# Optimization experiments

Measured on AMD Instinct MI355X. Metric: run time of the kernel, lower is better.

The kernel has to match this reference:

```python
import jax, jax.numpy as jnp
import numpy as np

CLAMP = 1000.0


def setup_inputs() -> dict:
    key = jax.random.key(0)
    k1, k2 = jax.random.split(key)
    B, C, H, W = 1, 32, 160, 320
    left = jax.random.normal(k1, (B, C, H, W), dtype=jnp.float32)
    right = jax.random.normal(k2, (B, C, H, W), dtype=jnp.float32)
    return {"left": left, "right": right, "num_disparities": 64}


def reference(left, right, num_disparities):
    # Left cost volume (is_right=False):
    #   out[b,c,d,h,w] = left[b,c,h,w] * right[b,c,h,w-d]  if w >= d else 0
    orig_dtype = left.dtype
    l = left.astype(jnp.float32)
    r = right.astype(jnp.float32)
    B, C, H, W = l.shape
    d = jnp.arange(num_disparities)[:, None]          # (D, 1)
    w = jnp.arange(W)[None, :]                        # (1, W)
    idx = w - d                                       # (D, W)
    valid = idx >= 0                                  # (D, W)
    # Gather shifted right features: (B, C, H, D, W) -> (B, C, D, H, W)
    rg = r[..., jnp.clip(idx, 0, W - 1)]
    rg = jnp.transpose(rg, (0, 1, 3, 2, 4))
    vol = l[:, :, None, :, :] * rg                    # (B, C, D, H, W)
    vol = jnp.where(valid[None, None, :, None, :], vol, jnp.float32(0))
    return jnp.clip(vol, -CLAMP, CLAMP).astype(orig_dtype)
```

## Files before the change

kernel.cpp:

```cpp
#include <hip/hip_runtime.h>


typedef float fx4 __attribute__((ext_vector_type(4)));

constexpr float CLAMPV = 1000.0f;
constexpr int C   = 32;
constexpr int H   = 160;
constexpr int W   = 320;
constexpr int W4  = 80;
constexpr int TH  = 4;
constexpr int BLOCK = TH * W4;
constexpr int PAD = 16;
constexpr int RS  = PAD + W4;

__device__ __forceinline__ fx4 clamp4(fx4 l, fx4 r) {
    fx4 o;
    o.x = fminf(fmaxf(l.x * r.x, -CLAMPV), CLAMPV);
    o.y = fminf(fmaxf(l.y * r.y, -CLAMPV), CLAMPV);
    o.z = fminf(fmaxf(l.z * r.z, -CLAMPV), CLAMPV);
    o.w = fminf(fmaxf(l.w * r.w, -CLAMPV), CLAMPV);
    return o;
}

template<int O>
__device__ __forceinline__ fx4 shuf(const fx4 A, const fx4 B) {
    if constexpr (O == 0) {
        return A;
    } else if constexpr (O == 1) {
        fx4 r = {A.y, A.z, A.w, B.x}; return r;
    } else if constexpr (O == 2) {
        fx4 r = {A.z, A.w, B.x, B.y}; return r;
    } else {
        fx4 r = {A.w, B.x, B.y, B.z}; return r;
    }
}

template<int C0>
__device__ __forceinline__ void group(const fx4* __restrict__ Ab, const fx4 l,
                                      float* __restrict__ ob, int w4, int D,
                                      size_t DSTRIDE) {
    constexpr int O = (4 - (C0 & 3)) & 3;
    const int kmax = (D - C0 + 3) >> 2;
    float* p = ob + (size_t)C0 * DSTRIDE;
    int qa = w4 - (C0 ? 1 : 0);
    for (int k = 0; k < kmax; ++k, --qa, p += 4 * DSTRIDE) {
        const fx4 A = Ab[qa];
        fx4 r;
        if constexpr (O == 0) {
            r = A;
        } else {
            const fx4 B = Ab[qa + 1];
            r = shuf<O>(A, B);
        }
        const fx4 o = clamp4(l, r);
        __builtin_nontemporal_store(o, reinterpret_cast<fx4*>(p));
    }
}

__global__ __launch_bounds__(BLOCK) void costvol_kernel(
    const float* __restrict__ left,
    const float* __restrict__ right,
    float* __restrict__ out,
    int D)
{
    const int blk = blockIdx.x;
    const int c   = blk / (H / TH);
    const int h0  = (blk - c * (H / TH)) * TH;

    __shared__ fx4 sR[TH * RS];

    const int t = threadIdx.x;
    const size_t inbase = ((size_t)c * H + h0) * W;
    const fx4* lg = reinterpret_cast<const fx4*>(left  + inbase);
    const fx4* rg = reinterpret_cast<const fx4*>(right + inbase);

    if (t < TH * PAD) {
        const int row = t / PAD, col = t - row * PAD;
        fx4 z = {0.f, 0.f, 0.f, 0.f};
        sR[row * RS + col] = z;
    }
    {
        const int row = t / W4, col = t - row * W4;
        sR[row * RS + PAD + col] = rg[t];
    }
    const fx4 l = lg[t];
    __syncthreads();

    const int h_ = t / W4;
    const int w4 = t - h_ * W4;
    const fx4* Ab = sR + h_ * RS + PAD;
    float* ob = out + ((size_t)c * D * H + h0) * W + 4 * (size_t)t;
    const size_t DSTRIDE = (size_t)H * W;

    group<0>(Ab, l, ob, w4, D, DSTRIDE);
    group<3>(Ab, l, ob, w4, D, DSTRIDE);
    group<2>(Ab, l, ob, w4, D, DSTRIDE);
    group<1>(Ab, l, ob, w4, D, DSTRIDE);
}

extern "C" void kernel_launch(void* const* d_in, const int* in_sizes, int n_in,
                              void* d_out, int out_size, void* d_ws, size_t ws_size,
                              hipStream_t stream) {
    const float* left  = (const float*)d_in[0];
    const float* right = (const float*)d_in[1];
    float* out = (float*)d_out;

    const int D = out_size / in_sizes[0];

    dim3 grid(C * (H / TH), 1, 1);
    dim3 block(BLOCK, 1, 1);
    costvol_kernel<<<grid, block, 0, stream>>>(left, right, out, D);
}
```

Before: 87.49 us.

## Assign one workgroup per (channel, disparity) plane with chunked row staging

```diff
diff --git a/kernel.cpp b/kernel.cpp
--- a/kernel.cpp
+++ b/kernel.cpp
@@ -4,14 +4,16 @@
 typedef float fx4 __attribute__((ext_vector_type(4)));
 
 constexpr float CLAMPV = 1000.0f;
-constexpr int C   = 32;
-constexpr int H   = 160;
-constexpr int W   = 320;
-constexpr int W4  = 80;
-constexpr int TH  = 4;
-constexpr int BLOCK = TH * W4;
+constexpr int C  = 32;
+constexpr int H  = 160;
+constexpr int W  = 320;
+constexpr int W4 = 80;
+constexpr int CH = 8;
 constexpr int PAD = 16;
 constexpr int RS  = PAD + W4;
+constexpr int BLOCK  = 256;
+constexpr int NCHUNK = H / CH;
+constexpr int CF4    = CH * W4;
 
 __device__ __forceinline__ fx4 clamp4(fx4 l, fx4 r) {
     fx4 o;
@@ -22,80 +24,83 @@
     return o;
 }
 
-template<int O>
-__device__ __forceinline__ fx4 shuf(const fx4 A, const fx4 B) {
-    if constexpr (O == 0) {
-        return A;
-    } else if constexpr (O == 1) {
-        fx4 r = {A.y, A.z, A.w, B.x}; return r;
-    } else if constexpr (O == 2) {
-        fx4 r = {A.z, A.w, B.x, B.y}; return r;
-    } else {
-        fx4 r = {A.w, B.x, B.y, B.z}; return r;
+template<int S>
+__device__ __forceinline__ void run(const float* __restrict__ lbase,
+                                    const float* __restrict__ rbase,
+                                    float* __restrict__ obase,
+                                    fx4* __restrict__ sR,
+                                    const int t, const int dq) {
+    for (int ck = 0; ck < NCHUNK; ++ck) {
+        const float* rrow = rbase + ck * CH * W;
+        if (t < CH * PAD) {
+            const int row = t >> 4, col = t & 15;
+            fx4 z = {0.f, 0.f, 0.f, 0.f};
+            sR[row * RS + col] = z;
+        }
+        #pragma unroll
+        for (int i = t; i < CF4; i += BLOCK) {
+            const int row = i / W4, col = i - row * W4;
+            sR[row * RS + PAD + col] =
+                reinterpret_cast<const fx4*>(rrow + row * W)[col];
+        }
+        __syncthreads();
+
+        const float* lrow = lbase + ck * CH * W;
+        float*       orow = obase + ck * CH * W;
+        #pragma unroll
+        for (int i = t; i < CF4; i += BLOCK) {
+            const int row = i / W4, w4 = i - row * W4;
+            const fx4 l = reinterpret_cast<const fx4*>(lrow + row * W)[w4];
+            const fx4* Ab = sR + row * RS + PAD;
+            const int qa = w4 - dq - (S ? 1 : 0);
+            const fx4 A = Ab[qa];
+            fx4 r;
+            if constexpr (S == 0) {
+                r = A;
+            } else {
+                const fx4 B = Ab[qa + 1];
+                if constexpr (S == 1)      { fx4 v = {A.w, B.x, B.y, B.z}; r = v; }
+                else if constexpr (S == 2) { fx4 v = {A.z, A.w, B.x, B.y}; r = v; }
+                else                       { fx4 v = {A.y, A.z, A.w, B.x}; r = v; }
+            }
+            const fx4 o = clamp4(l, r);
+            __builtin_nontemporal_store(o,
+                reinterpret_cast<fx4*>(orow + row * W + 4 * w4));
+        }
+        __syncthreads();
     }
 }
 
-template<int C0>
-__device__ __forceinline__ void group(const fx4* __restrict__ Ab, const fx4 l,
-                                      float* __restrict__ ob, int w4, int D,
-                                      size_t DSTRIDE) {
-    constexpr int O = (4 - (C0 & 3)) & 3;
-    const int kmax = (D - C0 + 3) >> 2;
-    float* p = ob + (size_t)C0 * DSTRIDE;
-    int qa = w4 - (C0 ? 1 : 0);
-    for (int k = 0; k < kmax; ++k, --qa, p += 4 * DSTRIDE) {
-        const fx4 A = Ab[qa];
-        fx4 r;
-        if constexpr (O == 0) {
-            r = A;
-        } else {
-            const fx4 B = Ab[qa + 1];
-            r = shuf<O>(A, B);
-        }
-        const fx4 o = clamp4(l, r);
-        __builtin_nontemporal_store(o, reinterpret_cast<fx4*>(p));
-    }
-}
-
-__global__ __launch_bounds__(BLOCK) void costvol_kernel(
+__global__ __launch_bounds__(BLOCK, 8) void costvol_kernel(
     const float* __restrict__ left,
     const float* __restrict__ right,
     float* __restrict__ out,
     int D)
 {
-    const int blk = blockIdx.x;
-    const int c   = blk / (H / TH);
-    const int h0  = (blk - c * (H / TH)) * TH;
+    __shared__ fx4 sR[CH * RS];
 
-    __shared__ fx4 sR[TH * RS];
+    int b = blockIdx.x;
+    const int nwg = gridDim.x;
+    if ((nwg & 7) == 0) {
+        const int cpx = nwg >> 3;
+        b = (b & 7) * cpx + (b >> 3);
+    }
 
+    const int c = b / D;
+    const int d = b - c * D;
     const int t = threadIdx.x;
-    const size_t inbase = ((size_t)c * H + h0) * W;
-    const fx4* lg = reinterpret_cast<const fx4*>(left  + inbase);
-    const fx4* rg = reinterpret_cast<const fx4*>(right + inbase);
 
-    if (t < TH * PAD) {
-        const int row = t / PAD, col = t - row * PAD;
-        fx4 z = {0.f, 0.f, 0.f, 0.f};
-        sR[row * RS + col] = z;
+    const float* lbase = left  + (size_t)c * H * W;
+    const float* rbase = right + (size_t)c * H * W;
+    float*       obase = out   + (size_t)b * H * W;
+
+    const int dq = d >> 2;
+    switch (d & 3) {
+        case 0: run<0>(lbase, rbase, obase, sR, t, dq); break;
+        case 1: run<1>(lbase, rbase, obase, sR, t, dq); break;
+        case 2: run<2>(lbase, rbase, obase, sR, t, dq); break;
+        default: run<3>(lbase, rbase, obase, sR, t, dq); break;
     }
-    {
-        const int row = t / W4, col = t - row * W4;
-        sR[row * RS + PAD + col] = rg[t];
-    }
-    const fx4 l = lg[t];
-    __syncthreads();
-
-    const int h_ = t / W4;
-    const int w4 = t - h_ * W4;
-    const fx4* Ab = sR + h_ * RS + PAD;
-    float* ob = out + ((size_t)c * D * H + h0) * W + 4 * (size_t)t;
-    const size_t DSTRIDE = (size_t)H * W;
-
-    group<0>(Ab, l, ob, w4, D, DSTRIDE);
-    group<3>(Ab, l, ob, w4, D, DSTRIDE);
-    group<2>(Ab, l, ob, w4, D, DSTRIDE);
-    group<1>(Ab, l, ob, w4, D, DSTRIDE);
 }
 
 extern "C" void kernel_launch(void* const* d_in, const int* in_sizes, int n_in,
@@ -107,7 +112,7 @@
 
     const int D = out_size / in_sizes[0];
 
-    dim3 grid(C * (H / TH), 1, 1);
+    dim3 grid(C * D, 1, 1);
     dim3 block(BLOCK, 1, 1);
     costvol_kernel<<<grid, block, 0, stream>>>(left, right, out, D);
 }
```

Measured after the change: 90.00 us. 1.03x slower.
